# Optimization experiments

Measured on AMD Instinct MI355X. Metric: run time of the kernel, lower is better.

## Reference

```python
import jax, jax.numpy as jnp
import numpy as np
import math

B, T, D = 2, 4096, 1024
HD = D // 2                      # head_dim
DEPTH = 12
LAMBDA_INIT = 0.8 - 0.6 * math.exp(-0.3 * DEPTH)
SCALING = HD ** -0.5
EPS = 1e-5


def setup_inputs() -> dict:
    key = jax.random.key(0)
    ks = jax.random.split(key, 11)
    f32 = jnp.float32
    return {
        "q": jax.random.normal(ks[0], (B, T, D), f32),
        "k": jax.random.normal(ks[1], (B, T, D), f32),
        "v": jax.random.normal(ks[2], (B, T, D), f32),
        "Wq": jax.random.normal(ks[3], (D, D), f32) * 0.02,
        "Wk": jax.random.normal(ks[4], (HD, D), f32) * 0.02,
        "Wv": jax.random.normal(ks[5], (D, D), f32) * 0.02,
        "Wo": jax.random.normal(ks[6], (D, D), f32) * 0.02,
        "lambda_q1": jax.random.normal(ks[7], (HD,), f32) * 0.1,
        "lambda_k1": jax.random.normal(ks[8], (HD,), f32) * 0.1,
        "lambda_q2": jax.random.normal(ks[9], (HD,), f32) * 0.1,
        "lambda_k2": jax.random.normal(ks[10], (HD,), f32) * 0.1,
    }


def reference(q, k, v, Wq, Wk, Wv, Wo, lambda_q1, lambda_k1, lambda_q2, lambda_k2):
    b, t, d = q.shape
    s = k.shape[1]
    # projections (Linear with no bias: x @ W.T)
    qp = (q @ Wq.T).reshape(b, t, 2, HD).transpose(0, 2, 1, 3) * SCALING  # [b,2,t,hd]
    kp = k @ Wk.T                                                          # [b,s,hd] (shared by both score heads)
    # dual score maps + softmax over src
    scores = jnp.einsum("bhtd,bsd->bhts", qp, kp)                          # [b,2,t,s]
    scores = jax.nn.softmax(scores.astype(jnp.float32), axis=-1).astype(qp.dtype)
    # lambda-weighted subtraction
    lam1 = jnp.exp(jnp.sum(lambda_q1 * lambda_k1))
    lam2 = jnp.exp(jnp.sum(lambda_q2 * lambda_k2))
    lam = lam1 - lam2 + LAMBDA_INIT
    attn_w = scores[:, 0] - lam * scores[:, 1]                             # [b,t,s]
    # value matmul
    vp = v @ Wv.T                                                          # [b,s,d]
    attn = jnp.einsum("bts,bsd->btd", attn_w, vp)                          # [b,t,d]
    # RMSNorm over last dim (2*head_dim == d), no affine
    rms = jax.lax.rsqrt(jnp.mean(jnp.square(attn), axis=-1, keepdims=True) + EPS)
    attn = attn * rms * (1.0 - LAMBDA_INIT)
    return attn @ Wo.T
```

## Files before the change

kernel.cpp:

```cpp
#include <hip/hip_runtime.h>
#include <stdint.h>
#include <stddef.h>

#define T_   4096
#define BT_  8192
#define SCALING_F      0.04419417382415922f
#define LAMBDA_INIT_F  0.7836057665316212f
#define ONE_MINUS_LI_F 0.2163942334683788f

typedef __attribute__((ext_vector_type(8))) short short8;
typedef __attribute__((ext_vector_type(4))) short short4v;
typedef __attribute__((ext_vector_type(4))) float f32x4;

__device__ __forceinline__ short f2bf(float f){
  uint32_t u = __float_as_uint(f);
  uint32_t r = (u + 0x7fffu + ((u >> 16) & 1u)) >> 16;
  return (short)(uint16_t)r;
}

__device__ __forceinline__ f32x4 mfma16(short8 a, short8 b, f32x4 c){
  return __builtin_amdgcn_mfma_f32_16x16x32_bf16(a, b, c, 0, 0, 0);
}

__device__ __forceinline__ void stage16(short* lds, const short* g){
  __builtin_amdgcn_global_load_lds(
      (const __attribute__((address_space(1))) void*)g,
      (__attribute__((address_space(3))) void*)lds, 16, 0, 0);
}

__global__ void k_cvt(const float* __restrict__ in, short* __restrict__ out, int n4){
  int i  = blockIdx.x*blockDim.x + threadIdx.x;
  int st = gridDim.x*blockDim.x;
  for (; i < n4; i += st){
    float4 v = ((const float4*)in)[i];
    short4v o;
    o.x = f2bf(v.x); o.y = f2bf(v.y); o.z = f2bf(v.z); o.w = f2bf(v.w);
    ((short4v*)out)[i] = o;
  }
}

template<int EPI>
__global__ __launch_bounds__(256, 3) void k_gemm(const short* __restrict__ A,
                                                 const short* __restrict__ Bm,
                                                 void* __restrict__ Cp, int ldc){
  __shared__ short As[128*32];
  __shared__ short Bs[128*32];
  const int tid = threadIdx.x;
  const int w = tid >> 6, l = tid & 63;
  const int m0 = blockIdx.x * 128;
  const int n0 = blockIdx.y * 128;
  const int wr = w >> 1, wc = w & 1;

  f32x4 acc[4][4] = {};

  const short* gA = A  + (size_t)(m0 + w*32 + (l>>2))*1024 + (l&3)*8;
  const short* gB = Bm + (size_t)(n0 + w*32 + (l>>2))*1024 + (l&3)*8;

  for (int k0 = 0; k0 < 1024; k0 += 32){
    stage16(As + w*1024,       gA + k0);
    stage16(As + w*1024 + 512, gA + 16*1024 + k0);
    stage16(Bs + w*1024,       gB + k0);
    stage16(Bs + w*1024 + 512, gB + 16*1024 + k0);
    __syncthreads();
    short8 aF[4], bF[4];
    #pragma unroll
    for (int i = 0; i < 4; i++){
      aF[i] = *(const short8*)&As[(wr*64 + i*16 + (l&15))*32 + (l>>4)*8];
      bF[i] = *(const short8*)&Bs[(wc*64 + i*16 + (l&15))*32 + (l>>4)*8];
    }
    #pragma unroll
    for (int i = 0; i < 4; i++)
      #pragma unroll
      for (int j = 0; j < 4; j++)
        acc[i][j] = mfma16(aF[i], bF[j], acc[i][j]);
    __syncthreads();
  }

  #pragma unroll
  for (int i = 0; i < 4; i++){
    #pragma unroll
    for (int j = 0; j < 4; j++){
      const size_t r0 = (size_t)m0 + wr*64 + i*16 + (l>>4)*4;
      const size_t c  = (size_t)n0 + wc*64 + j*16 + (l&15);
      #pragma unroll
      for (int rg = 0; rg < 4; rg++){
        float v = acc[i][j][rg];
        if (EPI == 2){
          ((float*)Cp)[(r0+rg)*(size_t)ldc + c] = v;
        } else {
          if (EPI == 1) v *= SCALING_F;
          ((short*)Cp)[(r0+rg)*(size_t)ldc + c] = f2bf(v);
        }
      }
    }
  }
}

__global__ __launch_bounds__(512, 2) void k_attn(
    const short* __restrict__ QP, const short* __restrict__ KP,
    const short* __restrict__ VPT,
    const float* __restrict__ lq1, const float* __restrict__ lk1,
    const float* __restrict__ lq2, const float* __restrict__ lk2,
    short* __restrict__ Ab)
{
  __shared__ short Ks[64*512];
  __shared__ short Qs[32*1024];
  __shared__ short Pl[2][32][72];
  __shared__ float lsum[8][16];
  __shared__ float rinv[2][32];
  __shared__ float ssq[8][32];

  int wg = blockIdx.x;
  wg = (wg & 7)*32 + (wg >> 3);
  const int b  = wg >> 7;
  const int t0 = (wg & 127) * 32;

  const int tid = threadIdx.x;
  const int w = tid >> 6, l = tid & 63;

  float s1 = 0.f, s2 = 0.f;
  #pragma unroll
  for (int i = 0; i < 8; i++){
    int idx = l*8 + i;
    s1 += lq1[idx]*lk1[idx];
    s2 += lq2[idx]*lk2[idx];
  }
  #pragma unroll
  for (int off = 1; off < 64; off <<= 1){
    s1 += __shfl_xor(s1, off, 64);
    s2 += __shfl_xor(s2, off, 64);
  }
  const float lam = __expf(s1) - __expf(s2) + LAMBDA_INIT_F;

  const int rc = w >> 1, h = rc >> 1, tch = rc & 1, scb = w & 1;

  f32x4 acc[4][8] = {};
  float lacc[4] = {0.f,0.f,0.f,0.f};

  const short* kpb = KP  + (size_t)(b*T_)*512;
  const short* vbp = VPT + (size_t)(w*128 + (l&15))*BT_ + (size_t)b*T_ + (l>>4)*8;

  const int jx = (l >> 4) ^ (l & 3);
  const int kx = (l >> 2) & 1;

  {
    const short* qsrc = QP + (size_t)(b*T_ + t0)*1024;
    #pragma unroll
    for (int j = 0; j < 4; j++){
      int r = w*4 + j;
      #pragma unroll
      for (int h2 = 0; h2 < 2; h2++)
        stage16(&Qs[r*1024 + h2*512],
                qsrc + (size_t)r*1024 + (h2*64 + (l ^ (r & 7)))*8);
    }
    #pragma unroll
    for (int j = 0; j < 8; j++)
      stage16(&Ks[(w*8 + j)*512], kpb + (size_t)(w*8 + j)*512 + ((l ^ j)*8));
  }
  __syncthreads();

  const short* qp0 = &Qs[(tch*16 + (l&15))*1024 + h*512 + jx*8];
  const short* kp0 = &Ks[(scb*32 + (l&15))*512 + jx*8];
  const short* kp1 = kp0 + 16*512;

  for (int st = 0; st < 64; st++){
    const int s0 = st*64;

    short8 varr[16];
    #pragma unroll
    for (int dc = 0; dc < 8; dc++)
      #pragma unroll
      for (int ks = 0; ks < 2; ks++)
        varr[dc*2 + ks] = *(const short8*)(vbp + (size_t)dc*16*BT_ + s0 + ks*32);
    __builtin_amdgcn_sched_barrier(0);

    f32x4 sa0 = {0.f,0.f,0.f,0.f}, sa1 = {0.f,0.f,0.f,0.f};
    #pragma unroll
    for (int kk = 0; kk < 16; kk++){
      const int ko = ((kk ^ kx) << 5);
      short8 qf = *(const short8*)(qp0 + ko);
      short8 b0 = *(const short8*)(kp0 + ko);
      short8 b1 = *(const short8*)(kp1 + ko);
      sa0 = mfma16(qf, b0, sa0);
      sa1 = mfma16(qf, b1, sa1);
    }

    #pragma unroll
    for (int rg = 0; rg < 4; rg++){
      float e0 = __expf(sa0[rg]);
      float e1 = __expf(sa1[rg]);
      lacc[rg] += e0 + e1;
      int row = tch*16 + (l>>4)*4 + rg;
      Pl[h][row][(2*scb+0)*16 + (l&15)] = f2bf(e0);
      Pl[h][row][(2*scb+1)*16 + (l&15)] = f2bf(e1);
    }

    asm volatile("s_waitcnt lgkmcnt(0)" ::: "memory");
    __builtin_amdgcn_s_barrier();

    if (st + 1 < 64){
      const short* ksrc = kpb + (size_t)((st+1)*64 + w*8)*512;
      #pragma unroll
      for (int j = 0; j < 8; j++)
        stage16(&Ks[(w*8 + j)*512], ksrc + (size_t)j*512 + ((l ^ j)*8));
    }

    #pragma unroll
    for (int ks = 0; ks < 2; ks++){
      short8 pa[4];
      #pragma unroll
      for (int rc2 = 0; rc2 < 4; rc2++)
        pa[rc2] = *(const short8*)&Pl[rc2>>1][(rc2&1)*16 + (l&15)][ks*32 + (l>>4)*8];
      #pragma unroll
      for (int dc = 0; dc < 8; dc++)
        #pragma unroll
        for (int rc2 = 0; rc2 < 4; rc2++)
          acc[rc2][dc] = mfma16(pa[rc2], varr[dc*2 + ks], acc[rc2][dc]);
    }

    __syncthreads();
  }

  #pragma unroll
  for (int off = 1; off < 16; off <<= 1)
    #pragma unroll
    for (int rg = 0; rg < 4; rg++) lacc[rg] += __shfl_xor(lacc[rg], off, 16);
  if ((l & 15) == 0){
    #pragma unroll
    for (int rg = 0; rg < 4; rg++) lsum[w][(l>>4)*4 + rg] = lacc[rg];
  }
  __syncthreads();
  if (tid < 64){
    int hh = tid >> 5, t = tid & 31;
    int rcc = hh*2 + (t >> 4), ric = t & 15;
    rinv[hh][t] = 1.0f / (lsum[rcc*2][ric] + lsum[rcc*2+1][ric]);
  }
  __syncthreads();

  float ps[2][4] = {};
  #pragma unroll
  for (int tc = 0; tc < 2; tc++){
    #pragma unroll
    for (int dc = 0; dc < 8; dc++){
      #pragma unroll
      for (int rg = 0; rg < 4; rg++){
        int t32 = tc*16 + (l>>4)*4 + rg;
        float o = acc[tc][dc][rg]*rinv[0][t32] - lam*acc[2+tc][dc][rg]*rinv[1][t32];
        ps[tc][rg] += o*o;
      }
    }
  }
  #pragma unroll
  for (int tc = 0; tc < 2; tc++)
    #pragma unroll
    for (int off = 1; off < 16; off <<= 1)
      #pragma unroll
      for (int rg = 0; rg < 4; rg++) ps[tc][rg] += __shfl_xor(ps[tc][rg], off, 16);
  if ((l & 15) == 0){
    #pragma unroll
    for (int tc = 0; tc < 2; tc++)
      #pragma unroll
      for (int rg = 0; rg < 4; rg++) ssq[w][tc*16 + (l>>4)*4 + rg] = ps[tc][rg];
  }
  __syncthreads();

  #pragma unroll
  for (int tc = 0; tc < 2; tc++){
    #pragma unroll
    for (int rg = 0; rg < 4; rg++){
      int t32 = tc*16 + (l>>4)*4 + rg;
      float tot = 0.f;
      #pragma unroll
      for (int w8 = 0; w8 < 8; w8++) tot += ssq[w8][t32];
      float scale = rsqrtf(tot*(1.0f/1024.0f) + 1e-5f) * ONE_MINUS_LI_F;
      short* orow = Ab + (size_t)(b*T_ + t0 + t32)*1024 + w*128 + (l&15);
      #pragma unroll
      for (int dc = 0; dc < 8; dc++){
        float o = acc[tc][dc][rg]*rinv[0][t32] - lam*acc[2+tc][dc][rg]*rinv[1][t32];
        orow[dc*16] = f2bf(o*scale);
      }
    }
  }
}

extern "C" void kernel_launch(void* const* d_in, const int* in_sizes, int n_in,
                              void* d_out, int out_size, void* d_ws, size_t ws_size,
                              hipStream_t stream){
  const float* q   = (const float*)d_in[0];
  const float* k   = (const float*)d_in[1];
  const float* v   = (const float*)d_in[2];
  const float* Wq  = (const float*)d_in[3];
  const float* Wk  = (const float*)d_in[4];
  const float* Wv  = (const float*)d_in[5];
  const float* Wo  = (const float*)d_in[6];
  const float* lq1 = (const float*)d_in[7];
  const float* lk1 = (const float*)d_in[8];
  const float* lq2 = (const float*)d_in[9];
  const float* lk2 = (const float*)d_in[10];

  short* ws   = (short*)d_ws;
  short* qb   = ws;
  short* kb   = qb  + (size_t)8192*1024;
  short* vb   = kb  + (size_t)8192*1024;
  short* Wqb  = vb  + (size_t)8192*1024;
  short* Wkb  = Wqb + (size_t)1024*1024;
  short* Wvb  = Wkb + (size_t)512*1024;
  short* Wob  = Wvb + (size_t)1024*1024;
  short* QPb  = Wob + (size_t)1024*1024;
  short* KPb  = QPb + (size_t)8192*1024;
  short* VPTb = KPb + (size_t)8192*512;
  short* Ab   = qb;

  auto cvt = [&](const float* in, short* out, size_t n){
    int n4 = (int)(n/4);
    int grid = (n4 + 255)/256; if (grid > 2048) grid = 2048;
    k_cvt<<<grid, 256, 0, stream>>>(in, out, n4);
  };
  cvt(q,  qb,  (size_t)8192*1024);
  cvt(k,  kb,  (size_t)8192*1024);
  cvt(v,  vb,  (size_t)8192*1024);
  cvt(Wq, Wqb, (size_t)1024*1024);
  cvt(Wk, Wkb, (size_t)512*1024);
  cvt(Wv, Wvb, (size_t)1024*1024);
  cvt(Wo, Wob, (size_t)1024*1024);

  k_gemm<1><<<dim3(64, 8), 256, 0, stream>>>(qb, Wqb, QPb, 1024);
  k_gemm<0><<<dim3(64, 4), 256, 0, stream>>>(kb, Wkb, KPb, 512);
  k_gemm<0><<<dim3(8, 64), 256, 0, stream>>>(Wvb, vb, VPTb, 8192);
  k_attn<<<dim3(256), 512, 0, stream>>>(QPb, KPb, VPTb, lq1, lk1, lq2, lk2, Ab);
  k_gemm<2><<<dim3(64, 8), 256, 0, stream>>>(Ab, Wob, d_out, 1024);
}
```

Before: 452.5 us.

## Batch fp32-to-bf16 conversions into one launch and tune attention MFMA scheduling

Merges the seven conversion kernels into a single launch that walks segment boundaries, cutting launch overhead and tail idle time between small kernels. In the attention kernel, the QK^T reduction is split into even and odd accumulators to break the MFMA dependency chain. The MFMA blocks are wrapped in s_setprio, and the lambda computation moves after the main loop so it stays off the critical prologue. The segment lookup adds per-element branching in the conversion kernel.

```diff
diff --git a/kernel.cpp b/kernel.cpp
--- a/kernel.cpp
+++ b/kernel.cpp
@@ -28,14 +28,26 @@
       (__attribute__((address_space(3))) void*)lds, 16, 0, 0);
 }
 
-__global__ void k_cvt(const float* __restrict__ in, short* __restrict__ out, int n4){
+struct CvtArgs {
+  const float* src[7];
+  short*       dst[7];
+  int          n4[7];
+  int          total4;
+};
+
+__global__ void k_cvt(CvtArgs a){
   int i  = blockIdx.x*blockDim.x + threadIdx.x;
   int st = gridDim.x*blockDim.x;
-  for (; i < n4; i += st){
-    float4 v = ((const float4*)in)[i];
+  for (; i < a.total4; i += st){
+    int seg = 0, off = i;
+    #pragma unroll
+    for (int s = 0; s < 6; s++){
+      if (off >= a.n4[seg]){ off -= a.n4[seg]; seg++; }
+    }
+    float4 v = ((const float4*)a.src[seg])[off];
     short4v o;
     o.x = f2bf(v.x); o.y = f2bf(v.y); o.z = f2bf(v.z); o.w = f2bf(v.w);
-    ((short4v*)out)[i] = o;
+    ((short4v*)a.dst[seg])[off] = o;
   }
 }
 
@@ -118,20 +130,6 @@
   const int tid = threadIdx.x;
   const int w = tid >> 6, l = tid & 63;
 
-  float s1 = 0.f, s2 = 0.f;
-  #pragma unroll
-  for (int i = 0; i < 8; i++){
-    int idx = l*8 + i;
-    s1 += lq1[idx]*lk1[idx];
-    s2 += lq2[idx]*lk2[idx];
-  }
-  #pragma unroll
-  for (int off = 1; off < 64; off <<= 1){
-    s1 += __shfl_xor(s1, off, 64);
-    s2 += __shfl_xor(s2, off, 64);
-  }
-  const float lam = __expf(s1) - __expf(s2) + LAMBDA_INIT_F;
-
   const int rc = w >> 1, h = rc >> 1, tch = rc & 1, scb = w & 1;
 
   f32x4 acc[4][8] = {};
@@ -174,16 +172,27 @@
         varr[dc*2 + ks] = *(const short8*)(vbp + (size_t)dc*16*BT_ + s0 + ks*32);
     __builtin_amdgcn_sched_barrier(0);
 
-    f32x4 sa0 = {0.f,0.f,0.f,0.f}, sa1 = {0.f,0.f,0.f,0.f};
-    #pragma unroll
-    for (int kk = 0; kk < 16; kk++){
-      const int ko = ((kk ^ kx) << 5);
-      short8 qf = *(const short8*)(qp0 + ko);
-      short8 b0 = *(const short8*)(kp0 + ko);
-      short8 b1 = *(const short8*)(kp1 + ko);
-      sa0 = mfma16(qf, b0, sa0);
-      sa1 = mfma16(qf, b1, sa1);
-    }
+    f32x4 sa0e = {0.f,0.f,0.f,0.f}, sa0o = {0.f,0.f,0.f,0.f};
+    f32x4 sa1e = {0.f,0.f,0.f,0.f}, sa1o = {0.f,0.f,0.f,0.f};
+    __builtin_amdgcn_s_setprio(1);
+    #pragma unroll
+    for (int kk = 0; kk < 16; kk += 2){
+      const int ko0 = ((kk ^ kx) << 5);
+      const int ko1 = (((kk + 1) ^ kx) << 5);
+      short8 qf0 = *(const short8*)(qp0 + ko0);
+      short8 b00 = *(const short8*)(kp0 + ko0);
+      short8 b10 = *(const short8*)(kp1 + ko0);
+      sa0e = mfma16(qf0, b00, sa0e);
+      sa1e = mfma16(qf0, b10, sa1e);
+      short8 qf1 = *(const short8*)(qp0 + ko1);
+      short8 b01 = *(const short8*)(kp0 + ko1);
+      short8 b11 = *(const short8*)(kp1 + ko1);
+      sa0o = mfma16(qf1, b01, sa0o);
+      sa1o = mfma16(qf1, b11, sa1o);
+    }
+    __builtin_amdgcn_s_setprio(0);
+    f32x4 sa0 = sa0e + sa0o;
+    f32x4 sa1 = sa1e + sa1o;
 
     #pragma unroll
     for (int rg = 0; rg < 4; rg++){
@@ -211,15 +220,31 @@
       #pragma unroll
       for (int rc2 = 0; rc2 < 4; rc2++)
         pa[rc2] = *(const short8*)&Pl[rc2>>1][(rc2&1)*16 + (l&15)][ks*32 + (l>>4)*8];
+      __builtin_amdgcn_s_setprio(1);
       #pragma unroll
       for (int dc = 0; dc < 8; dc++)
         #pragma unroll
         for (int rc2 = 0; rc2 < 4; rc2++)
           acc[rc2][dc] = mfma16(pa[rc2], varr[dc*2 + ks], acc[rc2][dc]);
+      __builtin_amdgcn_s_setprio(0);
     }
 
     __syncthreads();
   }
+
+  float s1 = 0.f, s2 = 0.f;
+  #pragma unroll
+  for (int i = 0; i < 8; i++){
+    int idx = l*8 + i;
+    s1 += lq1[idx]*lk1[idx];
+    s2 += lq2[idx]*lk2[idx];
+  }
+  #pragma unroll
+  for (int off = 1; off < 64; off <<= 1){
+    s1 += __shfl_xor(s1, off, 64);
+    s2 += __shfl_xor(s2, off, 64);
+  }
+  const float lam = __expf(s1) - __expf(s2) + LAMBDA_INIT_F;
 
   #pragma unroll
   for (int off = 1; off < 16; off <<= 1)
@@ -311,18 +336,16 @@
   short* VPTb = KPb + (size_t)8192*512;
   short* Ab   = qb;
 
-  auto cvt = [&](const float* in, short* out, size_t n){
-    int n4 = (int)(n/4);
-    int grid = (n4 + 255)/256; if (grid > 2048) grid = 2048;
-    k_cvt<<<grid, 256, 0, stream>>>(in, out, n4);
-  };
-  cvt(q,  qb,  (size_t)8192*1024);
-  cvt(k,  kb,  (size_t)8192*1024);
-  cvt(v,  vb,  (size_t)8192*1024);
-  cvt(Wq, Wqb, (size_t)1024*1024);
-  cvt(Wk, Wkb, (size_t)512*1024);
-  cvt(Wv, Wvb, (size_t)1024*1024);
-  cvt(Wo, Wob, (size_t)1024*1024);
+  CvtArgs ca;
+  ca.src[0]=q;  ca.dst[0]=qb;  ca.n4[0]=(8192*1024)/4;
+  ca.src[1]=k;  ca.dst[1]=kb;  ca.n4[1]=(8192*1024)/4;
+  ca.src[2]=v;  ca.dst[2]=vb;  ca.n4[2]=(8192*1024)/4;
+  ca.src[3]=Wq; ca.dst[3]=Wqb; ca.n4[3]=(1024*1024)/4;
+  ca.src[4]=Wk; ca.dst[4]=Wkb; ca.n4[4]=(512*1024)/4;
+  ca.src[5]=Wv; ca.dst[5]=Wvb; ca.n4[5]=(1024*1024)/4;
+  ca.src[6]=Wo; ca.dst[6]=Wob; ca.n4[6]=(1024*1024)/4;
+  ca.total4 = ca.n4[0]+ca.n4[1]+ca.n4[2]+ca.n4[3]+ca.n4[4]+ca.n4[5]+ca.n4[6];
+  k_cvt<<<2048, 256, 0, stream>>>(ca);
 
   k_gemm<1><<<dim3(64, 8), 256, 0, stream>>>(qb, Wqb, QPb, 1024);
   k_gemm<0><<<dim3(64, 4), 256, 0, stream>>>(kb, Wkb, KPb, 512);
```

Result: slower. 479.4 us (+6.0%).
